# Kernel tuning notes

Hardware: AMD Instinct MI355X
Metric: run time of the kernel (lower is better)

## Reference

```python
import jax, jax.numpy as jnp
import numpy as np

B, K, D, H, NIRREPS = 1024, 16, 1024, 16, 16  # batch, seq_len(=group n), input_dim, heads, n_irreps
HD = D // H


def setup_inputs() -> dict:
    key = jax.random.key(0)
    ks = jax.random.split(key, 10)
    s = 1.0 / np.sqrt(D)
    return {
        "x": jax.random.normal(ks[0], (B, K, D), jnp.float32),
        "projectors": jax.random.normal(ks[1], (NIRREPS, K, K), jnp.float32) * 0.25,
        "Wq": jax.random.normal(ks[2], (D, D), jnp.float32) * s,
        "bq": jnp.zeros((D,), jnp.float32),
        "Wk": jax.random.normal(ks[3], (D, D), jnp.float32) * s,
        "bk": jnp.zeros((D,), jnp.float32),
        "Wv": jax.random.normal(ks[4], (D, D), jnp.float32) * s,
        "bv": jnp.zeros((D,), jnp.float32),
        "Wo": jax.random.normal(ks[5], (D, D), jnp.float32) * s,
        "bo": jnp.zeros((D,), jnp.float32),
    }


def reference(x, projectors, Wq, bq, Wk, bk, Wv, bv, Wo, bo):
    b, k, d = x.shape
    hd = d // H
    # QKV projections -> [b, H, k, hd]
    def heads(t):
        return t.reshape(b, k, H, hd).transpose(0, 2, 1, 3)
    Q = heads(x @ Wq + bq)
    Kt = heads(x @ Wk + bk)
    V = heads(x @ Wv + bv)
    scale = jnp.asarray(1.0 / np.sqrt(hd), x.dtype)

    # Per-irrep: project Q/K/V along the seq axis with P, run masked-free softmax
    # attention on tiny k x k scores, accumulate over irreps (eval mode, no dropout).
    def body(acc, P):
        Qp = jnp.einsum('ij,bhjd->bhid', P, Q)
        Kp = jnp.einsum('ij,bhjd->bhid', P, Kt)
        Vp = jnp.einsum('ij,bhjd->bhid', P, V)
        scores = jnp.einsum('bhid,bhjd->bhij', Qp, Kp) * scale
        w = jax.nn.softmax(scores, axis=-1)
        return acc + jnp.einsum('bhij,bhjd->bhid', w, Vp), None

    total, _ = jax.lax.scan(body, jnp.zeros_like(V), projectors)
    # merge heads -> [b, k, d], then output projection
    out = total.transpose(0, 2, 1, 3).reshape(b, k, d) @ Wo + bo
    return out
```

## Files before the change

kernel.cpp:

```cpp
#include <hip/hip_runtime.h>


typedef unsigned short u16;
typedef unsigned int u32;
typedef __attribute__((ext_vector_type(8))) __bf16 bf16x8;
typedef __attribute__((ext_vector_type(4))) float f32x4;
typedef __attribute__((ext_vector_type(4))) u32 u32x4;
typedef __attribute__((ext_vector_type(4))) u16 u16x4;
typedef __attribute__((ext_vector_type(4))) float float4v;
typedef __attribute__((address_space(1))) void gvoid;
typedef __attribute__((address_space(3))) void svoid;

#define MFMA16(a, b, c) __builtin_amdgcn_mfma_f32_16x16x32_bf16(a, b, c, 0, 0, 0)

__device__ __forceinline__ u16 f2bf(float f) {
  u32 u = __builtin_bit_cast(u32, f);
  return (u16)((u + 0x7fffu + ((u >> 16) & 1u)) >> 16);
}
__device__ __forceinline__ float bf2f(u16 h) {
  u32 u = ((u32)h) << 16;
  return __builtin_bit_cast(float, u);
}
__device__ __forceinline__ float ld_bias(const void* p, int i, int isf32) {
  return isf32 ? ((const float*)p)[i] : bf2f(((const u16*)p)[i]);
}
__device__ __forceinline__ bf16x8 ld_frag(const u16* p) {
  u32x4 v = *reinterpret_cast<const u32x4*>(p);
  return __builtin_bit_cast(bf16x8, v);
}
__device__ __forceinline__ bf16x8 ld_frag_lo(const u16* p, int lane) {
  u32x4 v = {0u, 0u, 0u, 0u};
  if (lane < 32) v = *reinterpret_cast<const u32x4*>(p);
  return __builtin_bit_cast(bf16x8, v);
}
__device__ __forceinline__ void async16(const u16* g, u16* l) {
  __builtin_amdgcn_global_load_lds((gvoid*)g, (svoid*)l, 16, 0, 0);
}

__device__ __forceinline__ bf16x8 c2frag(f32x4 v, int lane) {
  const u32 p01 = ((u32)f2bf(v[1]) << 16) | (u32)f2bf(v[0]);
  const u32 p23 = ((u32)f2bf(v[3]) << 16) | (u32)f2bf(v[2]);
  const int base = (lane & 15) + ((lane & 16) << 1);
  u32x4 o;
  o[0] = (u32)__shfl((int)p01, base);
  o[1] = (u32)__shfl((int)p23, base);
  o[2] = (u32)__shfl((int)p01, base + 16);
  o[3] = (u32)__shfl((int)p23, base + 16);
  if (lane >= 32) o = (u32x4){0u, 0u, 0u, 0u};
  return __builtin_bit_cast(bf16x8, o);
}

__global__ __launch_bounds__(1024) void detect_dtype(const u32* __restrict__ x,
                                                     int* __restrict__ flag) {
  const int tid = threadIdx.x;
  int cnt = 0;
#pragma unroll
  for (int q = 0; q < 4; ++q) {
    const u32x4 v = ((const u32x4*)x)[q * 1024 + tid];
#pragma unroll
    for (int j = 0; j < 4; ++j) {
      const u32 e = (v[j] >> 23) & 0xffu;
      cnt += (e >= 64u && e <= 191u) ? 1 : 0;
    }
  }
  __shared__ int sred[16];
  for (int o = 32; o; o >>= 1) cnt += __shfl_down(cnt, o);
  if ((tid & 63) == 0) sred[tid >> 6] = cnt;
  __syncthreads();
  if (tid == 0) {
    int t = 0;
#pragma unroll
    for (int i = 0; i < 16; ++i) t += sred[i];
    flag[0] = (t > 8192) ? 1 : 0;
  }
}

__global__ __launch_bounds__(256) void convert_x(const void* __restrict__ src,
                                                 u16* __restrict__ dst,
                                                 const int* __restrict__ flag) {
  const int i4 = blockIdx.x * 256 + threadIdx.x;
  if (*flag) {
    const float4v v = ((const float4v*)src)[i4];
    u16x4 o;
#pragma unroll
    for (int j = 0; j < 4; ++j) o[j] = f2bf(v[j]);
    ((u16x4*)dst)[i4] = o;
  } else {
    ((u16x4*)dst)[i4] = ((const u16x4*)src)[i4];
  }
}

__global__ __launch_bounds__(256) void transpose_conv(
    const void* __restrict__ w0, const void* __restrict__ w1,
    const void* __restrict__ w2, const void* __restrict__ w3,
    u16* __restrict__ d0, u16* __restrict__ d1, u16* __restrict__ d2,
    u16* __restrict__ d3, const int* __restrict__ flag) {
  __shared__ u16 tile[32][33];
  const int z = blockIdx.z;
  const void* src = (z == 0) ? w0 : (z == 1) ? w1 : (z == 2) ? w2 : w3;
  u16* dst = (z == 0) ? d0 : (z == 1) ? d1 : (z == 2) ? d2 : d3;
  const int isf32 = *flag;
  const int tx = threadIdx.x & 31;
  const int ty = (threadIdx.x >> 5) * 4;
  const int bx = blockIdx.x * 32;
  const int by = blockIdx.y * 32;
#pragma unroll
  for (int r = 0; r < 4; ++r) {
    const int idx = (by + ty + r) * 1024 + bx + tx;
    tile[ty + r][tx] = isf32 ? f2bf(((const float*)src)[idx]) : ((const u16*)src)[idx];
  }
  __syncthreads();
#pragma unroll
  for (int r = 0; r < 4; ++r)
    dst[(bx + ty + r) * 1024 + by + tx] = tile[tx][ty + r];
}

template <int MODE, int BK>
__global__ __launch_bounds__(256) void gemm_kernel(
    const u16* __restrict__ X, const u16* __restrict__ Wt,
    const void* __restrict__ b0, const void* __restrict__ b1,
    const void* __restrict__ b2, void* __restrict__ o0, u16* __restrict__ o1,
    u16* __restrict__ o2, const int* __restrict__ flag) {
  constexpr int CPR = BK / 8;
  constexpr int NISS = BK / 16;
  constexpr int KH = BK / 32;
  __shared__ alignas(16) u16 As[128 * BK];
  __shared__ alignas(16) u16 Bs[128 * BK];
  const int tid = threadIdx.x;
  const int wave = tid >> 6, lane = tid & 63;
  const int m0 = blockIdx.y * 128, n0 = blockIdx.x * 128;
  const int wm = (wave >> 1) * 64, wn = (wave & 1) * 64;
  const int fr = lane & 15, fq = lane >> 4;
  const int isf32 = *flag;

  f32x4 acc[4][4] = {};

  const u16* gA[NISS];
  const u16* gB[NISS];
  u16* lA[NISS];
  u16* lB[NISS];
#pragma unroll
  for (int i = 0; i < NISS; ++i) {
    const int slot = i * 256 + tid;
    const int row = slot / CPR, ch = (slot % CPR) * 8;
    gA[i] = X + (m0 + row) * 1024 + ch;
    gB[i] = Wt + (n0 + row) * 1024 + ch;
    lA[i] = As + (i * 256 + wave * 64) * 8;
    lB[i] = Bs + (i * 256 + wave * 64) * 8;
  }
  const u16* aRd = As + (wm + fr) * BK + fq * 8;
  const u16* bRd = Bs + (wn + fr) * BK + fq * 8;

  for (int kb = 0; kb < 1024 / BK; ++kb) {
    const int ko = kb * BK;
    if (kb) __syncthreads();
#pragma unroll
    for (int i = 0; i < NISS; ++i) async16(gA[i] + ko, lA[i]);
#pragma unroll
    for (int i = 0; i < NISS; ++i) async16(gB[i] + ko, lB[i]);
    __syncthreads();
    bf16x8 af[4][KH], bfr[4][KH];
#pragma unroll
    for (int h = 0; h < KH; ++h)
#pragma unroll
      for (int t = 0; t < 4; ++t) {
        af[t][h] = ld_frag(aRd + t * 16 * BK + h * 32);
        bfr[t][h] = ld_frag(bRd + t * 16 * BK + h * 32);
      }
#pragma unroll
    for (int h = 0; h < KH; ++h)
#pragma unroll
      for (int i = 0; i < 4; ++i)
#pragma unroll
        for (int j = 0; j < 4; ++j) acc[i][j] = MFMA16(af[i][h], bfr[j][h], acc[i][j]);
  }

  const int c = fr, g = fq;
  if (MODE == 0) {
    const int q = n0 >> 10;
    const int nb = (n0 & 1023) + wn;
    const void* bp = (q == 0) ? b0 : ((q == 1) ? b1 : b2);
    u16* q0 = (u16*)o0;
#pragma unroll
    for (int tm = 0; tm < 4; ++tm) {
      const int mbase = m0 + wm + tm * 16;
      const int bidx = mbase >> 4;
#pragma unroll
      for (int tn = 0; tn < 4; ++tn) {
        const int nl = nb + tn * 16 + c;
        const int h = nl >> 6, d = nl & 63;
        const float bias = ld_bias(bp, nl, isf32);
        const int bh = bidx * 16 + h;
        if (q == 2) {
          u16x4 pk;
#pragma unroll
          for (int r = 0; r < 4; ++r) pk[r] = f2bf(acc[tm][tn][r] + bias);
          *reinterpret_cast<u16x4*>(&o2[(bh * 64 + d) * 16 + g * 4]) = pk;
        } else {
          u16* dstq = (q == 0) ? q0 : o1;
#pragma unroll
          for (int r = 0; r < 4; ++r) {
            const int j = g * 4 + r;
            dstq[(bh * 16 + j) * 64 + d] = f2bf(acc[tm][tn][r] + bias);
          }
        }
      }
    }
  } else {
#pragma unroll
    for (int tm = 0; tm < 4; ++tm) {
      const int m = m0 + wm + tm * 16 + g * 4;
#pragma unroll
      for (int tn = 0; tn < 4; ++tn) {
        const int n = n0 + wn + tn * 16 + c;
        const float bias = ld_bias(b0, n, isf32);
        if (isf32) {
#pragma unroll
          for (int r = 0; r < 4; ++r)
            ((float*)o0)[(m + r) * 1024 + n] = acc[tm][tn][r] + bias;
        } else {
#pragma unroll
          for (int r = 0; r < 4; ++r)
            ((u16*)o0)[(m + r) * 1024 + n] = f2bf(acc[tm][tn][r] + bias);
        }
      }
    }
  }
}

__global__ __launch_bounds__(256) void attn_kernel(
    const u16* __restrict__ Qb, const u16* __restrict__ Kb, const u16* __restrict__ Vt,
    const void* __restrict__ P, u16* __restrict__ Tb,
    const int* __restrict__ flag) {
  __shared__ alignas(16) u16 Pl[4096];
  __shared__ alignas(16) u16 Ptl[4096];
  const int tid = threadIdx.x;
  const int isf32 = *flag;
#pragma unroll
  for (int i = 0; i < 16; ++i) {
    const int idx = i * 256 + tid;
    const u16 v = isf32 ? f2bf(((const float*)P)[idx]) : ((const u16*)P)[idx];
    Pl[idx] = v;
    const int p = idx >> 8, rc = idx & 255, rr = rc >> 4, cc = rc & 15;
    Ptl[(p << 8) + (cc << 4) + rr] = v;
  }
  __syncthreads();

  const int wave = tid >> 6, lane = tid & 63;
  const int bh = blockIdx.x * 4 + wave;
  const int fr = lane & 15, fq = lane >> 4;

  const u16* qb = Qb + bh * 1024;
  const u16* kb = Kb + bh * 1024;
  const u16* vb = Vt + bh * 1024;

  const bf16x8 qf0 = ld_frag(qb + fr * 64 + fq * 8);
  const bf16x8 qf1 = ld_frag(qb + fr * 64 + 32 + fq * 8);
  const bf16x8 kf0 = ld_frag(kb + fr * 64 + fq * 8);
  const bf16x8 kf1 = ld_frag(kb + fr * 64 + 32 + fq * 8);
  f32x4 S = {0.f, 0.f, 0.f, 0.f};
  S = MFMA16(qf0, kf0, S);
  S = MFMA16(qf1, kf1, S);
#pragma unroll
  for (int r = 0; r < 4; ++r) S[r] *= 0.125f;
  const bf16x8 St = c2frag(S, lane);

  f32x4 Mt = {0.f, 0.f, 0.f, 0.f};
#pragma unroll 4
  for (int p = 0; p < 16; ++p) {
    const bf16x8 pl = ld_frag_lo(Pl + (p << 8) + fr * 16 + fq * 8, lane);
    const bf16x8 pt = ld_frag_lo(Ptl + (p << 8) + fr * 16 + fq * 8, lane);
    f32x4 z = {0.f, 0.f, 0.f, 0.f};
    const f32x4 ApT = MFMA16(St, pl, z);
    const f32x4 BpT = MFMA16(pl, c2frag(ApT, lane), z);
    float e[4], s = 0.f;
#pragma unroll
    for (int r = 0; r < 4; ++r) {
      e[r] = __expf(BpT[r]);
      s += e[r];
    }
    s += __shfl_xor(s, 16);
    s += __shfl_xor(s, 32);
    const float rs = __frcp_rn(s);
    f32x4 w;
#pragma unroll
    for (int r = 0; r < 4; ++r) w[r] = e[r] * rs;
    Mt = MFMA16(pt, c2frag(w, lane), Mt);
  }

  const bf16x8 mb = c2frag(Mt, lane);

  const int b = bh >> 4, h = bh & 15;
  u16* outp = Tb + (b * 16 + fr) * 1024 + h * 64;
#pragma unroll
  for (int dt = 0; dt < 4; ++dt) {
    const bf16x8 vf = ld_frag_lo(vb + (dt * 16 + fr) * 16 + fq * 8, lane);
    f32x4 z = {0.f, 0.f, 0.f, 0.f};
    const f32x4 ot = MFMA16(vf, mb, z);
    u16x4 pk;
#pragma unroll
    for (int r = 0; r < 4; ++r) pk[r] = f2bf(ot[r]);
    *reinterpret_cast<u16x4*>(&outp[dt * 16 + fq * 4]) = pk;
  }
}

extern "C" void kernel_launch(void* const* d_in, const int* in_sizes, int n_in,
                              void* d_out, int out_size, void* d_ws, size_t ws_size,
                              hipStream_t stream) {
  const void* x = d_in[0];
  const void* proj = d_in[1];
  const void* Wq = d_in[2];
  const void* bq = d_in[3];
  const void* Wk = d_in[4];
  const void* bk = d_in[5];
  const void* Wv = d_in[6];
  const void* bv = d_in[7];
  const void* Wo = d_in[8];
  const void* bo = d_in[9];

  char* ws = (char*)d_ws;
  int* flag = (int*)ws;          ws += 256;
  u16* WtQKV = (u16*)ws;         ws += (size_t)3072 * 1024 * 2;
  u16* WtO   = (u16*)ws;         ws += (size_t)1024 * 1024 * 2;
  u16* Xb    = (u16*)ws;         ws += (size_t)16384 * 1024 * 2;
  u16* Qbuf  = (u16*)ws;         ws += (size_t)16384 * 1024 * 2;
  u16* Kbuf  = (u16*)ws;         ws += (size_t)16384 * 1024 * 2;
  u16* Vtb   = (u16*)ws;         ws += (size_t)16384 * 1024 * 2;
  u16* Tbuf  = (u16*)ws;         ws += (size_t)16384 * 1024 * 2;

  detect_dtype<<<1, 1024, 0, stream>>>((const u32*)x, flag);
  convert_x<<<16384, 256, 0, stream>>>(x, Xb, flag);
  transpose_conv<<<dim3(32, 32, 4), 256, 0, stream>>>(
      Wq, Wk, Wv, Wo, WtQKV, WtQKV + 1024 * 1024, WtQKV + 2 * 1024 * 1024, WtO, flag);

  gemm_kernel<0, 64><<<dim3(24, 128), 256, 0, stream>>>(
      Xb, WtQKV, bq, bk, bv, Qbuf, Kbuf, Vtb, flag);
  attn_kernel<<<4096, 256, 0, stream>>>(Qbuf, Kbuf, Vtb, proj, Tbuf, flag);
  gemm_kernel<1, 32><<<dim3(8, 128), 256, 0, stream>>>(
      Tbuf, WtO, bo, nullptr, nullptr, d_out, nullptr, nullptr, flag);
}
```

Measured before the change: 400.1 us.

## Replace GEMMs with 256x256-tile double-buffered pipelined kernel with swizzled LDS

Replaces the 128x128 single-buffered GEMM with a 256x256-tile, 512-thread kernel. It double-buffers A/B tiles in 128KB of LDS, XOR-swizzles the LDS layout to avoid bank conflicts, and interleaves async global loads with MFMA phases using explicit barriers, waitcnts and setprio. It also remaps block IDs into XCD-aware groups for L2 locality. The aim is to hide global-load latency and raise MFMA utilisation in the QKV and output projections. In exchange it uses far more LDS and registers, has a hand-tuned schedule that is fragile, and launches fewer blocks (256 for the output GEMM).

```diff
diff --git a/kernel.cpp b/kernel.cpp
--- a/kernel.cpp
+++ b/kernel.cpp
@@ -115,117 +115,242 @@
     dst[(bx + ty + r) * 1024 + by + tx] = tile[tx][ty + r];
 }
 
-template <int MODE, int BK>
-__global__ __launch_bounds__(256) void gemm_kernel(
+template <int MODE>
+__global__ __launch_bounds__(512, 2) void gemm256(
     const u16* __restrict__ X, const u16* __restrict__ Wt,
     const void* __restrict__ b0, const void* __restrict__ b1,
     const void* __restrict__ b2, void* __restrict__ o0, u16* __restrict__ o1,
     u16* __restrict__ o2, const int* __restrict__ flag) {
-  constexpr int CPR = BK / 8;
-  constexpr int NISS = BK / 16;
-  constexpr int KH = BK / 32;
-  __shared__ alignas(16) u16 As[128 * BK];
-  __shared__ alignas(16) u16 Bs[128 * BK];
+  __shared__ alignas(16) u16 sm[65536];
   const int tid = threadIdx.x;
   const int wave = tid >> 6, lane = tid & 63;
-  const int m0 = blockIdx.y * 128, n0 = blockIdx.x * 128;
-  const int wm = (wave >> 1) * 64, wn = (wave & 1) * 64;
   const int fr = lane & 15, fq = lane >> 4;
+  const int wm = wave >> 2, wn = wave & 3;
   const int isf32 = *flag;
 
-  f32x4 acc[4][4] = {};
-
-  const u16* gA[NISS];
-  const u16* gB[NISS];
-  u16* lA[NISS];
-  u16* lB[NISS];
-#pragma unroll
-  for (int i = 0; i < NISS; ++i) {
-    const int slot = i * 256 + tid;
-    const int row = slot / CPR, ch = (slot % CPR) * 8;
-    gA[i] = X + (m0 + row) * 1024 + ch;
-    gB[i] = Wt + (n0 + row) * 1024 + ch;
-    lA[i] = As + (i * 256 + wave * 64) * 8;
-    lB[i] = Bs + (i * 256 + wave * 64) * 8;
-  }
-  const u16* aRd = As + (wm + fr) * BK + fq * 8;
-  const u16* bRd = Bs + (wn + fr) * BK + fq * 8;
-
-  for (int kb = 0; kb < 1024 / BK; ++kb) {
-    const int ko = kb * BK;
-    if (kb) __syncthreads();
-#pragma unroll
-    for (int i = 0; i < NISS; ++i) async16(gA[i] + ko, lA[i]);
-#pragma unroll
-    for (int i = 0; i < NISS; ++i) async16(gB[i] + ko, lB[i]);
-    __syncthreads();
-    bf16x8 af[4][KH], bfr[4][KH];
-#pragma unroll
-    for (int h = 0; h < KH; ++h)
-#pragma unroll
-      for (int t = 0; t < 4; ++t) {
-        af[t][h] = ld_frag(aRd + t * 16 * BK + h * 32);
-        bfr[t][h] = ld_frag(bRd + t * 16 * BK + h * 32);
-      }
-#pragma unroll
-    for (int h = 0; h < KH; ++h)
-#pragma unroll
-      for (int i = 0; i < 4; ++i)
-#pragma unroll
-        for (int j = 0; j < 4; ++j) acc[i][j] = MFMA16(af[i][h], bfr[j][h], acc[i][j]);
-  }
-
-  const int c = fr, g = fq;
-  if (MODE == 0) {
+  const int nwg = gridDim.x;
+  const int per = nwg >> 3;
+  const int bid = blockIdx.x;
+  const int wg = (bid & 7) * per + (bid >> 3);
+  const int m0 = (wg & 63) << 8;
+  const int n0 = (wg >> 6) << 8;
+
+  const int gl = ((tid & 7) ^ ((tid >> 3) & 7)) * 8;
+  const u16* aS = X + (size_t)(m0 + (tid >> 3)) * 1024 + gl;
+  const u16* bS = Wt + (size_t)(n0 + (tid >> 3)) * 1024 + gl;
+  u16* dA = sm + wave * 512;
+  u16* dB = sm + 16384 + wave * 512;
+
+  const u16* aR = sm + (wm * 128 + fr) * 64;
+  const u16* bR = sm + 16384 + (wn * 64 + fr) * 64;
+  const int g0 = (fq ^ (fr & 7)) * 8;
+  const int g1 = ((fq ^ (fr & 7)) ^ 4) * 8;
+
+  f32x4 acc[2][4][4] = {};
+  bf16x8 af[2][4][2], bf[4][2];
+
+#define STG_A(BUF, H, KT)                                                     \
+  do {                                                                        \
+    async16(aS + (H * 128) * 1024 + (KT), dA + (BUF)*32768 + (H)*8192);       \
+    async16(aS + (H * 128 + 64) * 1024 + (KT),                                \
+            dA + (BUF)*32768 + (H)*8192 + 4096);                              \
+  } while (0)
+#define STG_B(BUF, H, KT)                                                     \
+  do {                                                                        \
+    async16(bS + (H * 128) * 1024 + (KT), dB + (BUF)*32768 + (H)*8192);       \
+    async16(bS + (H * 128 + 64) * 1024 + (KT),                                \
+            dB + (BUF)*32768 + (H)*8192 + 4096);                              \
+  } while (0)
+#define LDA_ALL(CH, KH, BUF)                                                  \
+  do {                                                                        \
+    af[CH][0][KH] = ld_frag(aR + (BUF)*32768 + (CH)*4096 + ((KH) ? g1 : g0)); \
+    af[CH][1][KH] =                                                           \
+        ld_frag(aR + (BUF)*32768 + (CH)*4096 + 1024 + ((KH) ? g1 : g0));      \
+    af[CH][2][KH] =                                                           \
+        ld_frag(aR + (BUF)*32768 + (CH)*4096 + 2048 + ((KH) ? g1 : g0));      \
+    af[CH][3][KH] =                                                           \
+        ld_frag(aR + (BUF)*32768 + (CH)*4096 + 3072 + ((KH) ? g1 : g0));      \
+  } while (0)
+#define LDB_ALL(KH, BUF)                                                      \
+  do {                                                                        \
+    bf[0][KH] = ld_frag(bR + (BUF)*32768 + ((KH) ? g1 : g0));                 \
+    bf[1][KH] = ld_frag(bR + (BUF)*32768 + 1024 + ((KH) ? g1 : g0));          \
+    bf[2][KH] = ld_frag(bR + (BUF)*32768 + 2048 + ((KH) ? g1 : g0));          \
+    bf[3][KH] = ld_frag(bR + (BUF)*32768 + 3072 + ((KH) ? g1 : g0));          \
+  } while (0)
+#define MM1(CH, FI, KH)                                                       \
+  acc[CH][FI][0] = MFMA16(af[CH][FI][KH], bf[0][KH], acc[CH][FI][0]);         \
+  acc[CH][FI][1] = MFMA16(af[CH][FI][KH], bf[1][KH], acc[CH][FI][1]);         \
+  acc[CH][FI][2] = MFMA16(af[CH][FI][KH], bf[2][KH], acc[CH][FI][2]);         \
+  acc[CH][FI][3] = MFMA16(af[CH][FI][KH], bf[3][KH], acc[CH][FI][3]);
+#define MM(CH, KH)                                                            \
+  do {                                                                        \
+    __builtin_amdgcn_s_setprio(1);                                            \
+    MM1(CH, 0, KH) MM1(CH, 1, KH) MM1(CH, 2, KH) MM1(CH, 3, KH)               \
+    __builtin_amdgcn_s_setprio(0);                                            \
+  } while (0)
+#define BARR                                                                  \
+  __builtin_amdgcn_s_barrier();                                               \
+  __builtin_amdgcn_sched_barrier(0)
+#define WAITV(N) asm volatile("s_waitcnt vmcnt(" #N ")" ::: "memory")
+#define WAITL asm volatile("s_waitcnt lgkmcnt(0)" ::: "memory")
+#define SCHED __builtin_amdgcn_sched_barrier(0)
+
+  STG_A(0, 0, 0);
+  STG_A(0, 1, 0);
+  STG_B(0, 0, 0);
+  STG_B(0, 1, 0);
+  STG_A(1, 0, 64);
+  STG_A(1, 1, 64);
+  WAITV(4);
+  BARR;
+
+  for (int it = 0; it < 7; ++it) {
+    const int kof = it * 128;
+    LDA_ALL(0, 0, 0);
+    LDB_ALL(0, 0);
+    LDA_ALL(1, 0, 0);
+    STG_B(1, 0, kof + 64);
+    BARR;
+    MM(0, 0);
+    BARR;
+    LDA_ALL(0, 1, 0);
+    LDA_ALL(1, 1, 0);
+    STG_B(1, 1, kof + 64);
+    BARR;
+    MM(1, 0);
+    WAITL;
+    SCHED;
+    BARR;
+    LDB_ALL(1, 0);
+    STG_A(0, 0, kof + 128);
+    BARR;
+    MM(0, 1);
+    BARR;
+    STG_A(0, 1, kof + 128);
+    BARR;
+    MM(1, 1);
+    WAITV(4);
+    SCHED;
+    BARR;
+    LDA_ALL(0, 0, 1);
+    LDB_ALL(0, 1);
+    LDA_ALL(1, 0, 1);
+    STG_B(0, 0, kof + 128);
+    BARR;
+    MM(0, 0);
+    BARR;
+    LDA_ALL(0, 1, 1);
+    LDA_ALL(1, 1, 1);
+    STG_B(0, 1, kof + 128);
+    BARR;
+    MM(1, 0);
+    WAITL;
+    SCHED;
+    BARR;
+    LDB_ALL(1, 1);
+    STG_A(1, 0, kof + 192);
+    BARR;
+    MM(0, 1);
+    BARR;
+    STG_A(1, 1, kof + 192);
+    BARR;
+    MM(1, 1);
+    WAITV(4);
+    SCHED;
+    BARR;
+  }
+
+  {
+    LDA_ALL(0, 0, 0);
+    LDB_ALL(0, 0);
+    LDA_ALL(1, 0, 0);
+    LDA_ALL(0, 1, 0);
+    LDA_ALL(1, 1, 0);
+    LDB_ALL(1, 0);
+    STG_B(1, 0, 960);
+    STG_B(1, 1, 960);
+    MM(0, 0);
+    MM(1, 0);
+    MM(0, 1);
+    MM(1, 1);
+    WAITV(0);
+    BARR;
+    LDA_ALL(0, 0, 1);
+    LDB_ALL(0, 1);
+    LDA_ALL(1, 0, 1);
+    LDA_ALL(0, 1, 1);
+    LDA_ALL(1, 1, 1);
+    LDB_ALL(1, 1);
+    MM(0, 0);
+    MM(1, 0);
+    MM(0, 1);
+    MM(1, 1);
+  }
+
+  if constexpr (MODE == 0) {
     const int q = n0 >> 10;
-    const int nb = (n0 & 1023) + wn;
+    const int nb = (n0 & 1023) + wn * 64;
     const void* bp = (q == 0) ? b0 : ((q == 1) ? b1 : b2);
     u16* q0 = (u16*)o0;
 #pragma unroll
-    for (int tm = 0; tm < 4; ++tm) {
-      const int mbase = m0 + wm + tm * 16;
-      const int bidx = mbase >> 4;
-#pragma unroll
-      for (int tn = 0; tn < 4; ++tn) {
-        const int nl = nb + tn * 16 + c;
-        const int h = nl >> 6, d = nl & 63;
-        const float bias = ld_bias(bp, nl, isf32);
-        const int bh = bidx * 16 + h;
-        if (q == 2) {
-          u16x4 pk;
-#pragma unroll
-          for (int r = 0; r < 4; ++r) pk[r] = f2bf(acc[tm][tn][r] + bias);
-          *reinterpret_cast<u16x4*>(&o2[(bh * 64 + d) * 16 + g * 4]) = pk;
-        } else {
-          u16* dstq = (q == 0) ? q0 : o1;
-#pragma unroll
-          for (int r = 0; r < 4; ++r) {
-            const int j = g * 4 + r;
-            dstq[(bh * 16 + j) * 64 + d] = f2bf(acc[tm][tn][r] + bias);
+    for (int ch = 0; ch < 2; ++ch)
+#pragma unroll
+      for (int fi = 0; fi < 4; ++fi) {
+        const int mbase = m0 + wm * 128 + ch * 64 + fi * 16;
+        const int bidx = mbase >> 4;
+#pragma unroll
+        for (int bj = 0; bj < 4; ++bj) {
+          const int nl = nb + bj * 16 + fr;
+          const int h = nl >> 6, d = nl & 63;
+          const float bias = ld_bias(bp, nl, isf32);
+          const int bh = bidx * 16 + h;
+          if (q == 2) {
+            u16x4 pk;
+#pragma unroll
+            for (int r = 0; r < 4; ++r) pk[r] = f2bf(acc[ch][fi][bj][r] + bias);
+            *reinterpret_cast<u16x4*>(&o2[(bh * 64 + d) * 16 + fq * 4]) = pk;
+          } else {
+            u16* dstq = (q == 0) ? q0 : o1;
+#pragma unroll
+            for (int r = 0; r < 4; ++r)
+              dstq[(bh * 16 + fq * 4 + r) * 64 + d] =
+                  f2bf(acc[ch][fi][bj][r] + bias);
           }
         }
       }
-    }
   } else {
 #pragma unroll
-    for (int tm = 0; tm < 4; ++tm) {
-      const int m = m0 + wm + tm * 16 + g * 4;
-#pragma unroll
-      for (int tn = 0; tn < 4; ++tn) {
-        const int n = n0 + wn + tn * 16 + c;
-        const float bias = ld_bias(b0, n, isf32);
-        if (isf32) {
-#pragma unroll
-          for (int r = 0; r < 4; ++r)
-            ((float*)o0)[(m + r) * 1024 + n] = acc[tm][tn][r] + bias;
-        } else {
-#pragma unroll
-          for (int r = 0; r < 4; ++r)
-            ((u16*)o0)[(m + r) * 1024 + n] = f2bf(acc[tm][tn][r] + bias);
+    for (int ch = 0; ch < 2; ++ch)
+#pragma unroll
+      for (int fi = 0; fi < 4; ++fi) {
+        const int m = m0 + wm * 128 + ch * 64 + fi * 16 + fq * 4;
+#pragma unroll
+        for (int bj = 0; bj < 4; ++bj) {
+          const int n = n0 + wn * 64 + bj * 16 + fr;
+          const float bias = ld_bias(b0, n, isf32);
+          if (isf32) {
+#pragma unroll
+            for (int r = 0; r < 4; ++r)
+              ((float*)o0)[(m + r) * 1024 + n] = acc[ch][fi][bj][r] + bias;
+          } else {
+#pragma unroll
+            for (int r = 0; r < 4; ++r)
+              ((u16*)o0)[(m + r) * 1024 + n] = f2bf(acc[ch][fi][bj][r] + bias);
+          }
         }
       }
-    }
-  }
+  }
+#undef STG_A
+#undef STG_B
+#undef LDA_ALL
+#undef LDB_ALL
+#undef MM1
+#undef MM
+#undef BARR
+#undef WAITV
+#undef WAITL
+#undef SCHED
 }
 
 __global__ __launch_bounds__(256) void attn_kernel(
@@ -333,9 +458,9 @@
   transpose_conv<<<dim3(32, 32, 4), 256, 0, stream>>>(
       Wq, Wk, Wv, Wo, WtQKV, WtQKV + 1024 * 1024, WtQKV + 2 * 1024 * 1024, WtO, flag);
 
-  gemm_kernel<0, 64><<<dim3(24, 128), 256, 0, stream>>>(
+  gemm256<0><<<dim3(768), 512, 0, stream>>>(
       Xb, WtQKV, bq, bk, bv, Qbuf, Kbuf, Vtb, flag);
   attn_kernel<<<4096, 256, 0, stream>>>(Qbuf, Kbuf, Vtb, proj, Tbuf, flag);
-  gemm_kernel<1, 32><<<dim3(8, 128), 256, 0, stream>>>(
+  gemm256<1><<<dim3(256), 512, 0, stream>>>(
       Tbuf, WtO, bo, nullptr, nullptr, d_out, nullptr, nullptr, flag);
 }
```

After: 362.4 us. -9.4%, faster.
